# Kernel tuning notes

Measured on AMD Instinct MI355X. Metric: run time of the kernel, lower is better.

The kernel has to match this reference:

```python
import jax, jax.numpy as jnp
import numpy as np

GAMMA = 2.2
EPS = 1e-08


def _up2(x):
    B, C, H, W = x.shape
    return jax.image.resize(x, (B, C, 2 * H, 2 * W), method='bilinear')


def _pixel_unshuffle2(x):
    # [B,1,2H,2W] -> [B,4,H,W], torch channel order (ry, rx)
    B, C, H2, W2 = x.shape
    H, W = H2 // 2, W2 // 2
    x = x.reshape(B, C, H, 2, W, 2)
    x = x.transpose(0, 1, 3, 5, 2, 4)
    return x.reshape(B, C * 4, H, W)


def _pixel_shuffle2(x):
    # [B,4,H,W] -> [B,1,2H,2W]
    B, C4, H, W = x.shape
    C = C4 // 4
    x = x.reshape(B, C, 2, 2, H, W)
    x = x.transpose(0, 1, 4, 2, 5, 3)
    return x.reshape(B, C, 2 * H, 2 * W)


def _demosaic(bayer):
    # bayer: [B,4,H,W] packed RGGB planes -> [B,3,2H,2W]
    red = _up2(bayer[:, 0:1])

    gr = jnp.flip(bayer[:, 1:2], axis=-1)
    gr = jnp.flip(_up2(gr), axis=-1)
    gr = _pixel_unshuffle2(gr)  # [B,4,H,W]

    gb = jnp.flip(bayer[:, 2:3], axis=-2)
    gb = jnp.flip(_up2(gb), axis=-2)
    gb = _pixel_unshuffle2(gb)  # [B,4,H,W]

    green = jnp.stack([
        (gr[:, 0] + gb[:, 0]) * 0.5,  # green at red site
        gr[:, 1],                      # green at green-red site
        gb[:, 2],                      # green at green-blue site
        (gr[:, 3] + gb[:, 3]) * 0.5,  # green at blue site
    ], axis=1)
    green = _pixel_shuffle2(green)  # [B,1,2H,2W]

    blue = jnp.flip(bayer[:, 3:4], axis=-1)
    blue = jnp.flip(_up2(blue), axis=-1)

    return jnp.concatenate([red, green, blue], axis=1)


def _isp(x, awb_gains, ccms):
    if x.shape[1] == 4:
        x = _demosaic(x)
    x = x * 2.0
    x = x[:, ::-1]  # channel order [2,1,0]
    x = jnp.einsum('bchw,bck->bkhw', x, awb_gains)  # awb_en=1, clip=0
    x = jnp.einsum('bchw,bck->bkhw', x, ccms)       # ccm_en=1, clip=0
    x = x[:, ::-1]
    # gamma compression
    return jnp.clip(x, EPS) ** jnp.float32(1.0 / GAMMA)


def setup_inputs() -> dict:
    key = jax.random.key(0)
    k1, k2, k3, k4, k5 = jax.random.split(key, 5)
    B, H, W = 8, 512, 512
    return {
        'pred': jax.random.uniform(k1, (B, 4, H, W), dtype=jnp.float32),
        'gt': jax.random.uniform(k2, (B, 4, H, W), dtype=jnp.float32),
        'awb': jax.random.uniform(k3, (B, 3, 3), dtype=jnp.float32),
        'cam2rgb': jax.random.uniform(k4, (B, 3, 3), dtype=jnp.float32),
        'rgb_gain': jax.random.uniform(k5, (B,), dtype=jnp.float32),
    }


def reference(pred, gt, awb, cam2rgb, rgb_gain):
    # rgb_gain (dgain) is accepted but unused, matching the torch module.
    x = _isp(pred, awb, cam2rgb)
    y = _isp(gt, awb, cam2rgb)
    return (x, y)
```

## Files before the change

kernel.cpp:

```cpp
#include <hip/hip_runtime.h>


#define GAMMA_INV 0.45454545454545453f
#define EPS_CLIP 1e-8f

__device__ __forceinline__ float gamma_enc(float v) {
  v = fmaxf(v, EPS_CLIP);
  return exp2f(GAMMA_INV * __log2f(v));
}

__device__ __forceinline__ void load_row(const float* __restrict__ row,
                                         int im, int i, int ip, float w[6]) {
  float4 v = *reinterpret_cast<const float4*>(row + i);
  w[0] = row[im];
  w[1] = v.x; w[2] = v.y; w[3] = v.z; w[4] = v.w;
  w[5] = row[ip];
}

__device__ __forceinline__ void up2_row4(const float* __restrict__ ch,
                                         int jm, int j, int jp,
                                         int im, int i, int ip,
                                         float top[8], float bot[8]) {
  const int W = 512;
  float w0[6], w1[6], w2[6];
  load_row(ch + jm * W, im, i, ip, w0);
  load_row(ch + j  * W, im, i, ip, w1);
  load_row(ch + jp * W, im, i, ip, w2);
  float e[6], o[6];
#pragma unroll
  for (int c = 0; c < 6; ++c) {
    e[c] = 0.25f * w0[c] + 0.75f * w1[c];
    o[c] = 0.75f * w1[c] + 0.25f * w2[c];
  }
#pragma unroll
  for (int p = 0; p < 4; ++p) {
    int wp = p + 1;
    top[2 * p]     = 0.25f * e[wp - 1] + 0.75f * e[wp];
    top[2 * p + 1] = 0.75f * e[wp]     + 0.25f * e[wp + 1];
    bot[2 * p]     = 0.25f * o[wp - 1] + 0.75f * o[wp];
    bot[2 * p + 1] = 0.75f * o[wp]     + 0.25f * o[wp + 1];
  }
}

__global__ __launch_bounds__(256) void isp_kernel(
    const float* __restrict__ pred, const float* __restrict__ gt,
    const float* __restrict__ awb, const float* __restrict__ ccm,
    float* __restrict__ out) {
  constexpr int H = 512, W = 512;
  constexpr int HW = H * W;
  constexpr long long OUT_IMG = 8LL * 3 * 1024 * 1024;

  int idx = blockIdx.x * blockDim.x + threadIdx.x;
  int t   = idx & 127;
  int j   = (idx >> 7) & 511;
  int b   = (idx >> 16) & 7;
  int img = idx >> 19;

  const float* A  = awb + b * 9;
  const float* Cm = ccm + b * 9;
  float M[3][3];
#pragma unroll
  for (int k = 0; k < 3; ++k) {
#pragma unroll
    for (int e = 0; e < 3; ++e) {
      int ar = (2 - e) * 3;
      int cc = 2 - k;
      M[k][e] = 2.0f * (A[ar + 0] * Cm[0 + cc] +
                        A[ar + 1] * Cm[3 + cc] +
                        A[ar + 2] * Cm[6 + cc]);
    }
  }

  int i  = 4 * t;
  int jm = (j > 0) ? j - 1 : 0;
  int jp = (j < H - 1) ? j + 1 : H - 1;
  int im = (i > 0) ? i - 1 : 0;
  int ip = (i + 4 < W) ? i + 4 : W - 1;

  const float* src = (img ? gt : pred) + (long long)b * 4 * HW;

  float rT[8], rB[8], gT[8], gB[8], bT[8], bB[8];
  float tT[8], tB[8];

  up2_row4(src + 0 * HW, jm, j, jp, im, i, ip, rT, rB);
  up2_row4(src + 1 * HW, jm, j, jp, im, i, ip, gT, gB);
  up2_row4(src + 2 * HW, jm, j, jp, im, i, ip, tT, tB);
#pragma unroll
  for (int p = 0; p < 4; ++p) {
    gT[2 * p]     = 0.5f * (gT[2 * p] + tT[2 * p]);
    gB[2 * p]     = tB[2 * p];
    gB[2 * p + 1] = 0.5f * (gB[2 * p + 1] + tB[2 * p + 1]);
  }
  up2_row4(src + 3 * HW, jm, j, jp, im, i, ip, bT, bB);

  int oy = 2 * j, ox = 8 * t;
  float* dst = out + (long long)img * OUT_IMG;

#pragma unroll
  for (int k = 0; k < 3; ++k) {
    float oT[8], oB[8];
#pragma unroll
    for (int p = 0; p < 8; ++p) {
      oT[p] = gamma_enc(M[k][0] * rT[p] + M[k][1] * gT[p] + M[k][2] * bT[p]);
      oB[p] = gamma_enc(M[k][0] * rB[p] + M[k][1] * gB[p] + M[k][2] * bB[p]);
    }
    long long obase = ((long long)(b * 3 + k) * 1024 + oy) * 1024 + ox;
    *reinterpret_cast<float4*>(dst + obase)          = make_float4(oT[0], oT[1], oT[2], oT[3]);
    *reinterpret_cast<float4*>(dst + obase + 4)      = make_float4(oT[4], oT[5], oT[6], oT[7]);
    *reinterpret_cast<float4*>(dst + obase + 1024)     = make_float4(oB[0], oB[1], oB[2], oB[3]);
    *reinterpret_cast<float4*>(dst + obase + 1028)     = make_float4(oB[4], oB[5], oB[6], oB[7]);
  }
}

extern "C" void kernel_launch(void* const* d_in, const int* in_sizes, int n_in,
                              void* d_out, int out_size, void* d_ws, size_t ws_size,
                              hipStream_t stream) {
  const float* pred = (const float*)d_in[0];
  const float* gt   = (const float*)d_in[1];
  const float* awb  = (const float*)d_in[2];
  const float* ccm  = (const float*)d_in[3];
  float* out = (float*)d_out;

  const int total = 2 * 8 * 512 * 128;
  dim3 block(256);
  dim3 grid(total / 256);
  isp_kernel<<<grid, block, 0, stream>>>(pred, gt, awb, ccm, out);
}
```

Baseline: 271.0 us.

## Process 8 input columns per thread with wave shuffles for halos and nontemporal stores

Each thread now handles 8 input pixels per row instead of 4, so one 64-lane wavefront covers a full 512-wide row. The left and right halo values come from neighbouring lanes via shuffles, replacing scalar global loads, and clamped edges are handled at lanes 0 and 63. Output writes use nontemporal vector stores to avoid polluting the cache with the large write stream. The thread count halves and per-thread register use roughly doubles, which may reduce occupancy.

```diff
diff --git a/kernel.cpp b/kernel.cpp
--- a/kernel.cpp
+++ b/kernel.cpp
@@ -4,42 +4,50 @@
 #define GAMMA_INV 0.45454545454545453f
 #define EPS_CLIP 1e-8f
 
+typedef float f32x4 __attribute__((ext_vector_type(4)));
+
 __device__ __forceinline__ float gamma_enc(float v) {
   v = fmaxf(v, EPS_CLIP);
   return exp2f(GAMMA_INV * __log2f(v));
 }
 
-__device__ __forceinline__ void load_row(const float* __restrict__ row,
-                                         int im, int i, int ip, float w[6]) {
-  float4 v = *reinterpret_cast<const float4*>(row + i);
-  w[0] = row[im];
-  w[1] = v.x; w[2] = v.y; w[3] = v.z; w[4] = v.w;
-  w[5] = row[ip];
-}
-
-__device__ __forceinline__ void up2_row4(const float* __restrict__ ch,
-                                         int jm, int j, int jp,
-                                         int im, int i, int ip,
-                                         float top[8], float bot[8]) {
+__device__ __forceinline__ void up2_row8(const float* __restrict__ ch,
+                                         int jm, int j, int jp, int i, int lane,
+                                         float top[16], float bot[16]) {
   const int W = 512;
-  float w0[6], w1[6], w2[6];
-  load_row(ch + jm * W, im, i, ip, w0);
-  load_row(ch + j  * W, im, i, ip, w1);
-  load_row(ch + jp * W, im, i, ip, w2);
-  float e[6], o[6];
+  const float* r0 = ch + jm * W + i;
+  const float* r1 = ch + j  * W + i;
+  const float* r2 = ch + jp * W + i;
+  f32x4 a0 = *reinterpret_cast<const f32x4*>(r0);
+  f32x4 a1 = *reinterpret_cast<const f32x4*>(r0 + 4);
+  f32x4 b0 = *reinterpret_cast<const f32x4*>(r1);
+  f32x4 b1 = *reinterpret_cast<const f32x4*>(r1 + 4);
+  f32x4 c0 = *reinterpret_cast<const f32x4*>(r2);
+  f32x4 c1 = *reinterpret_cast<const f32x4*>(r2 + 4);
+  float A[8]  = {a0.x, a0.y, a0.z, a0.w, a1.x, a1.y, a1.z, a1.w};
+  float Bv[8] = {b0.x, b0.y, b0.z, b0.w, b1.x, b1.y, b1.z, b1.w};
+  float Cv[8] = {c0.x, c0.y, c0.z, c0.w, c1.x, c1.y, c1.z, c1.w};
+  float e[8], o[8];
 #pragma unroll
-  for (int c = 0; c < 6; ++c) {
-    e[c] = 0.25f * w0[c] + 0.75f * w1[c];
-    o[c] = 0.75f * w1[c] + 0.25f * w2[c];
+  for (int c = 0; c < 8; ++c) {
+    e[c] = 0.25f * A[c]  + 0.75f * Bv[c];
+    o[c] = 0.75f * Bv[c] + 0.25f * Cv[c];
   }
+  float eL = __shfl_up(e[7], 1);   eL = (lane == 0)  ? e[0] : eL;
+  float oL = __shfl_up(o[7], 1);   oL = (lane == 0)  ? o[0] : oL;
+  float eR = __shfl_down(e[0], 1); eR = (lane == 63) ? e[7] : eR;
+  float oR = __shfl_down(o[0], 1); oR = (lane == 63) ? o[7] : oR;
+  top[0] = 0.25f * eL + 0.75f * e[0];
+  bot[0] = 0.25f * oL + 0.75f * o[0];
 #pragma unroll
-  for (int p = 0; p < 4; ++p) {
-    int wp = p + 1;
-    top[2 * p]     = 0.25f * e[wp - 1] + 0.75f * e[wp];
-    top[2 * p + 1] = 0.75f * e[wp]     + 0.25f * e[wp + 1];
-    bot[2 * p]     = 0.25f * o[wp - 1] + 0.75f * o[wp];
-    bot[2 * p + 1] = 0.75f * o[wp]     + 0.25f * o[wp + 1];
+  for (int p = 0; p < 7; ++p) {
+    top[2 * p + 1] = 0.75f * e[p] + 0.25f * e[p + 1];
+    top[2 * p + 2] = 0.25f * e[p] + 0.75f * e[p + 1];
+    bot[2 * p + 1] = 0.75f * o[p] + 0.25f * o[p + 1];
+    bot[2 * p + 2] = 0.25f * o[p] + 0.75f * o[p + 1];
   }
+  top[15] = 0.75f * e[7] + 0.25f * eR;
+  bot[15] = 0.75f * o[7] + 0.25f * oR;
 }
 
 __global__ __launch_bounds__(256) void isp_kernel(
@@ -50,11 +58,12 @@
   constexpr int HW = H * W;
   constexpr long long OUT_IMG = 8LL * 3 * 1024 * 1024;
 
-  int idx = blockIdx.x * blockDim.x + threadIdx.x;
-  int t   = idx & 127;
-  int j   = (idx >> 7) & 511;
-  int b   = (idx >> 16) & 7;
-  int img = idx >> 19;
+  int idx  = blockIdx.x * blockDim.x + threadIdx.x;
+  int tg   = idx & 63;
+  int j    = (idx >> 6) & 511;
+  int b    = (idx >> 15) & 7;
+  int img  = idx >> 18;
+  int lane = tg;
 
   const float* A  = awb + b * 9;
   const float* Cm = ccm + b * 9;
@@ -71,44 +80,43 @@
     }
   }
 
-  int i  = 4 * t;
+  int i  = 8 * tg;
   int jm = (j > 0) ? j - 1 : 0;
   int jp = (j < H - 1) ? j + 1 : H - 1;
-  int im = (i > 0) ? i - 1 : 0;
-  int ip = (i + 4 < W) ? i + 4 : W - 1;
 
   const float* src = (img ? gt : pred) + (long long)b * 4 * HW;
 
-  float rT[8], rB[8], gT[8], gB[8], bT[8], bB[8];
-  float tT[8], tB[8];
+  float rT[16], rB[16], gT[16], gB[16], qT[16], qB[16];
+  up2_row8(src + 0 * HW, jm, j, jp, i, lane, rT, rB);
+  up2_row8(src + 1 * HW, jm, j, jp, i, lane, gT, gB);
+  up2_row8(src + 2 * HW, jm, j, jp, i, lane, qT, qB);
+#pragma unroll
+  for (int p = 0; p < 8; ++p) {
+    gT[2 * p]     = 0.5f * (gT[2 * p] + qT[2 * p]);
+    gB[2 * p]     = qB[2 * p];
+    gB[2 * p + 1] = 0.5f * (gB[2 * p + 1] + qB[2 * p + 1]);
+  }
+  up2_row8(src + 3 * HW, jm, j, jp, i, lane, qT, qB);
 
-  up2_row4(src + 0 * HW, jm, j, jp, im, i, ip, rT, rB);
-  up2_row4(src + 1 * HW, jm, j, jp, im, i, ip, gT, gB);
-  up2_row4(src + 2 * HW, jm, j, jp, im, i, ip, tT, tB);
-#pragma unroll
-  for (int p = 0; p < 4; ++p) {
-    gT[2 * p]     = 0.5f * (gT[2 * p] + tT[2 * p]);
-    gB[2 * p]     = tB[2 * p];
-    gB[2 * p + 1] = 0.5f * (gB[2 * p + 1] + tB[2 * p + 1]);
-  }
-  up2_row4(src + 3 * HW, jm, j, jp, im, i, ip, bT, bB);
-
-  int oy = 2 * j, ox = 8 * t;
+  int oy = 2 * j, ox = 16 * tg;
   float* dst = out + (long long)img * OUT_IMG;
 
 #pragma unroll
   for (int k = 0; k < 3; ++k) {
-    float oT[8], oB[8];
+    float oT[16], oB[16];
 #pragma unroll
-    for (int p = 0; p < 8; ++p) {
-      oT[p] = gamma_enc(M[k][0] * rT[p] + M[k][1] * gT[p] + M[k][2] * bT[p]);
-      oB[p] = gamma_enc(M[k][0] * rB[p] + M[k][1] * gB[p] + M[k][2] * bB[p]);
+    for (int p = 0; p < 16; ++p) {
+      oT[p] = gamma_enc(M[k][0] * rT[p] + M[k][1] * gT[p] + M[k][2] * qT[p]);
+      oB[p] = gamma_enc(M[k][0] * rB[p] + M[k][1] * gB[p] + M[k][2] * qB[p]);
     }
     long long obase = ((long long)(b * 3 + k) * 1024 + oy) * 1024 + ox;
-    *reinterpret_cast<float4*>(dst + obase)          = make_float4(oT[0], oT[1], oT[2], oT[3]);
-    *reinterpret_cast<float4*>(dst + obase + 4)      = make_float4(oT[4], oT[5], oT[6], oT[7]);
-    *reinterpret_cast<float4*>(dst + obase + 1024)     = make_float4(oB[0], oB[1], oB[2], oB[3]);
-    *reinterpret_cast<float4*>(dst + obase + 1028)     = make_float4(oB[4], oB[5], oB[6], oB[7]);
+#pragma unroll
+    for (int q = 0; q < 4; ++q) {
+      f32x4 vT = {oT[4 * q], oT[4 * q + 1], oT[4 * q + 2], oT[4 * q + 3]};
+      f32x4 vB = {oB[4 * q], oB[4 * q + 1], oB[4 * q + 2], oB[4 * q + 3]};
+      __builtin_nontemporal_store(vT, reinterpret_cast<f32x4*>(dst + obase + 4 * q));
+      __builtin_nontemporal_store(vB, reinterpret_cast<f32x4*>(dst + obase + 1024 + 4 * q));
+    }
   }
 }
 
@@ -121,7 +129,7 @@
   const float* ccm  = (const float*)d_in[3];
   float* out = (float*)d_out;
 
-  const int total = 2 * 8 * 512 * 128;
+  const int total = 2 * 8 * 512 * 64;
   dim3 block(256);
   dim3 grid(total / 256);
   isp_kernel<<<grid, block, 0, stream>>>(pred, gt, awb, ccm, out);
```

Measured after the change: 487.8 us. 1.8x slower.
